# Kernel tuning notes

Measured on AMD Instinct MI355X. Metric: run time of the kernel, lower is better.

The kernel has to match this reference:

```python
import jax, jax.numpy as jnp
import numpy as np

B, N, D = 8, 8192, 256
H, DK, M, DH = 8, 32, 64, 512   # heads, per-head key dim, n_omega random features, mlp hidden
DV = D // H                      # per-head value dim
EPS = 1e-3                       # keras LayerNormalization default epsilon


def _layer_norm(x, g, b):
    mu = jnp.mean(x, axis=-1, keepdims=True)
    var = jnp.var(x, axis=-1, keepdims=True)
    return g * (x - mu) * jax.lax.rsqrt(var + EPS) + b


def _phi(x, omega):
    # Performer positive random features. x: (B,H,N,DK), omega: (DK,M)
    x = x / (DK ** 0.25)
    proj = jnp.einsum('bhnd,dm->bhnm', x, omega)
    sq = 0.5 * jnp.sum(x * x, axis=-1, keepdims=True)
    return jnp.exp(proj - sq) / jnp.sqrt(jnp.asarray(M, x.dtype))


def _mhla(x, Wq, bq, Wk, bk, Wv, bv, Wo, bo, omega):
    # x: (B,N,D). Multi-head linear (kernelized) attention.
    q = (x @ Wq + bq).reshape(B, N, H, DK).transpose(0, 2, 1, 3)  # bhnd
    k = (x @ Wk + bk).reshape(B, N, H, DK).transpose(0, 2, 1, 3)
    v = (x @ Wv + bv).reshape(B, N, H, DV).transpose(0, 2, 1, 3)
    pq = _phi(q, omega)                                   # (B,H,N,M)
    pk = _phi(k, omega)                                   # (B,H,N,M)
    kv = jnp.einsum('bhnm,bhnd->bhmd', pk, v)             # (B,H,M,DV)
    num = jnp.einsum('bhnm,bhmd->bhnd', pq, kv)           # (B,H,N,DV)
    den = jnp.einsum('bhnm,bhm->bhn', pq, jnp.sum(pk, axis=2))
    out = num / den[..., None]
    out = out.transpose(0, 2, 1, 3).reshape(B, N, D)
    return out @ Wo + bo


def _gru_gate(x, y, Wr, Ur, Wz, Uz, Wg, Ug, bg):
    # GTrXL gating: x = residual (old state), y = new sublayer output.
    r = jax.nn.sigmoid(y @ Wr + x @ Ur)
    z = jax.nn.sigmoid(y @ Wz + x @ Uz - bg)
    h = jnp.tanh(y @ Wg + (r * x) @ Ug)
    return (1.0 - z) * x + z * h


def setup_inputs() -> dict:
    key = jax.random.key(0)
    ks = iter(jax.random.split(key, 40))
    w = lambda *s: jax.random.normal(next(ks), s, jnp.float32) * 0.02
    inp = {
        'x': jax.random.normal(next(ks), (B, N, D), jnp.float32),
        'ln1_g': jnp.ones((D,), jnp.float32), 'ln1_b': jnp.zeros((D,), jnp.float32),
        'Wq': w(D, H * DK), 'bq': jnp.zeros((H * DK,), jnp.float32),
        'Wk': w(D, H * DK), 'bk': jnp.zeros((H * DK,), jnp.float32),
        'Wv': w(D, H * DV), 'bv': jnp.zeros((H * DV,), jnp.float32),
        'Wo': w(D, D), 'bo': jnp.zeros((D,), jnp.float32),
        'omega': jax.random.normal(next(ks), (DK, M), jnp.float32),
        'g1_Wr': w(D, D), 'g1_Ur': w(D, D), 'g1_Wz': w(D, D), 'g1_Uz': w(D, D),
        'g1_Wg': w(D, D), 'g1_Ug': w(D, D), 'g1_bg': 2.0 * jnp.ones((D,), jnp.float32),
        'ln2_g': jnp.ones((D,), jnp.float32), 'ln2_b': jnp.zeros((D,), jnp.float32),
        'W1': w(D, DH), 'b1': jnp.zeros((DH,), jnp.float32),
        'W2': w(DH, D), 'b2': jnp.zeros((D,), jnp.float32),
        'g2_Wr': w(D, D), 'g2_Ur': w(D, D), 'g2_Wz': w(D, D), 'g2_Uz': w(D, D),
        'g2_Wg': w(D, D), 'g2_Ug': w(D, D), 'g2_bg': 2.0 * jnp.ones((D,), jnp.float32),
    }
    return inp


def reference(x, ln1_g, ln1_b, Wq, bq, Wk, bk, Wv, bv, Wo, bo, omega,
              g1_Wr, g1_Ur, g1_Wz, g1_Uz, g1_Wg, g1_Ug, g1_bg,
              ln2_g, ln2_b, W1, b1, W2, b2,
              g2_Wr, g2_Ur, g2_Wz, g2_Uz, g2_Wg, g2_Ug, g2_bg):
    residual = x
    h = _layer_norm(x, ln1_g, ln1_b)
    h = _mhla(h, Wq, bq, Wk, bk, Wv, bv, Wo, bo, omega)
    h = _gru_gate(residual, h, g1_Wr, g1_Ur, g1_Wz, g1_Uz, g1_Wg, g1_Ug, g1_bg)
    residual = h
    h2 = _layer_norm(h, ln2_g, ln2_b)
    h2 = jax.nn.relu(h2 @ W1 + b1)
    h2 = jax.nn.relu(h2 @ W2 + b2)
    out = _gru_gate(residual, h2, g2_Wr, g2_Ur, g2_Wz, g2_Uz, g2_Wg, g2_Ug, g2_bg)
    return out
```

## Files before the change

### kernel.cpp

```cpp
#include <hip/hip_runtime.h>

#define B_ 8
#define N_ 8192
#define H_ 8
#define KSPLIT 16
#define BN 65536

typedef float f32x4 __attribute__((ext_vector_type(4)));
typedef __bf16 bf16x8 __attribute__((ext_vector_type(8)));
typedef unsigned short u16;

__device__ __forceinline__ u16 f2b(float f) {
  union { float f; unsigned u; } v; v.f = f;
  return (u16)((v.u + 0x7fffu + ((v.u >> 16) & 1u)) >> 16);
}
__device__ __forceinline__ float b2f(u16 u) {
  union { unsigned u; float f; } v; v.u = ((unsigned)u) << 16;
  return v.f;
}

__device__ __forceinline__ void gload16(const void* g, const void* lds) {
  __builtin_amdgcn_global_load_lds(
      (const __attribute__((address_space(1))) unsigned int*)(unsigned long long)g,
      (__attribute__((address_space(3))) unsigned int*)(unsigned long long)lds,
      16, 0, 0);
}

__device__ __forceinline__ void ld16f(const float* p, float* f) {
#pragma unroll
  for (int j = 0; j < 4; ++j) {
    float4 q = *(const float4*)(p + j * 4);
    f[j * 4 + 0] = q.x; f[j * 4 + 1] = q.y; f[j * 4 + 2] = q.z; f[j * 4 + 3] = q.w;
  }
}
__device__ __forceinline__ void ld16b(const u16* p, float* f) {
  uint4 a = *(const uint4*)p, b = *(const uint4*)(p + 8);
  const unsigned uu[8] = {a.x, a.y, a.z, a.w, b.x, b.y, b.z, b.w};
#pragma unroll
  for (int j = 0; j < 8; ++j) {
    f[2 * j]     = b2f((u16)(uu[j] & 0xffff));
    f[2 * j + 1] = b2f((u16)(uu[j] >> 16));
  }
}
__device__ __forceinline__ void st16b(u16* p, const float* f) {
  u16 o[16];
#pragma unroll
  for (int j = 0; j < 16; ++j) o[j] = f2b(f[j]);
  *(uint4*)p = *(const uint4*)o;
  *(uint4*)(p + 8) = *(const uint4*)(o + 8);
}
__device__ __forceinline__ void st16f(float* p, const float* f) {
#pragma unroll
  for (int j = 0; j < 4; ++j) {
    float4 q; q.x = f[j * 4]; q.y = f[j * 4 + 1]; q.z = f[j * 4 + 2]; q.w = f[j * 4 + 3];
    *(float4*)(p + j * 4) = q;
  }
}

template <int MODE, int XBF, int CF32, int BSEL>
__global__ __launch_bounds__(512) void gemm2(
    const u16* __restrict__ A1, int lda1, const u16* __restrict__ A2, int lda2,
    const u16* __restrict__ BT, int ldb,
    const float* __restrict__ bias, const void* __restrict__ auxX,
    const u16* __restrict__ auxZ, const float* __restrict__ auxS,
    void* __restrict__ Cv, void* __restrict__ Cv2, void* __restrict__ Cv3,
    int ldc, int K) {
  __shared__ __align__(16) u16 As[3][4096];
  __shared__ __align__(16) u16 Bs[3][8192];
  const int t = threadIdx.x, lane = t & 63, w = t >> 6;
  const int nwg = gridDim.x * gridDim.y;
  const int flat = blockIdx.x + gridDim.x * blockIdx.y;
  const int wg = (flat & 7) * (nwg >> 3) + (flat >> 3);
  const int bx = wg % gridDim.x, by = wg / gridDim.x;
  const int rowBase = by * 128, colBase = bx * 256;
  const int aBase = (BSEL == 2) ? (rowBase & 255) : rowBase;
  const u16* BTb = BT;
  if (BSEL == 1) BTb = BT + (size_t)(rowBase >> 13) * 131072;
  if (BSEL == 2) BTb = BT + (size_t)(rowBase >> 8) * 131072;

  const int lr = lane & 15, kg = lane >> 4;
  const int wrow = (w >> 2) * 64, wcol = (w & 3) * 64;

  f32x4 acc[4][4];
#pragma unroll
  for (int m = 0; m < 4; ++m)
#pragma unroll
    for (int n = 0; n < 4; ++n) acc[m][n] = 0.f;

  const int nt = K >> 5;
  auto stage = [&](int s) {
    const int buf = s % 3;
    const int k0 = s << 5;
    const u16* Ap; int la, ka;
    if (k0 < 256) { Ap = A1; la = lda1; ka = k0; }
    else          { Ap = A2; la = lda2; ka = k0 - 256; }
    {
      int row = t >> 2, sl = t & 3;
      int ks = (sl ^ ((row & 6) >> 1)) * 8;
      gload16(&Ap[(size_t)(aBase + row) * la + ka + ks], &As[buf][t * 8]);
    }
#pragma unroll
    for (int j = 0; j < 2; ++j) {
      int slot = j * 512 + t;
      int col = slot >> 2, sl = slot & 3;
      int ks = (sl ^ ((col & 6) >> 1)) * 8;
      gload16(&BTb[(size_t)(colBase + col) * ldb + k0 + ks], &Bs[buf][slot * 8]);
    }
  };

  auto lbar = [&]() {
    asm volatile("s_waitcnt lgkmcnt(0)" ::: "memory");
    __builtin_amdgcn_sched_barrier(0);
    __builtin_amdgcn_s_barrier();
    __builtin_amdgcn_sched_barrier(0);
  };

  stage(0);
  stage(1);
  for (int s = 0; s < nt; ++s) {
    const int buf = s % 3;
    if (nt - s > 1) asm volatile("s_waitcnt vmcnt(3)" ::: "memory");
    else            asm volatile("s_waitcnt vmcnt(0)" ::: "memory");
    __builtin_amdgcn_sched_barrier(0);
    __builtin_amdgcn_s_barrier();
    __builtin_amdgcn_sched_barrier(0);
    if (s + 2 < nt) stage(s + 2);
    bf16x8 af[4], bf[4];
#pragma unroll
    for (int m = 0; m < 4; ++m) {
      int row = wrow + m * 16 + lr;
      af[m] = *(const bf16x8*)&As[buf][row * 32 + (kg ^ ((row & 6) >> 1)) * 8];
    }
#pragma unroll
    for (int n = 0; n < 4; ++n) {
      int col = wcol + n * 16 + lr;
      bf[n] = *(const bf16x8*)&Bs[buf][col * 32 + (kg ^ ((col & 6) >> 1)) * 8];
    }
    __builtin_amdgcn_s_setprio(1);
#pragma unroll
    for (int m = 0; m < 4; ++m)
#pragma unroll
      for (int n = 0; n < 4; ++n)
        acc[m][n] = __builtin_amdgcn_mfma_f32_16x16x32_bf16(af[m], bf[n], acc[m][n], 0, 0, 0);
    __builtin_amdgcn_s_setprio(0);
  }

  lbar();
  float* scr = (float*)&Bs[0][0];
#pragma unroll
  for (int m = 0; m < 4; ++m) {
    if (m) lbar();
#pragma unroll
    for (int n = 0; n < 4; ++n)
#pragma unroll
      for (int i = 0; i < 4; ++i)
        scr[((w >> 2) * 16 + kg * 4 + i) * 260 + wcol + n * 16 + lr] = acc[m][n][i];
    lbar();
    const int sr = t >> 4, cs = (t & 15) * 16;
    const int grow = rowBase + (sr >> 4) * 64 + m * 16 + (sr & 15);
    const int gcol = colBase + cs;
    float vv[16];
#pragma unroll
    for (int j = 0; j < 4; ++j) {
      float4 q = *(const float4*)&scr[sr * 260 + cs + j * 4];
      vv[j * 4] = q.x; vv[j * 4 + 1] = q.y; vv[j * 4 + 2] = q.z; vv[j * 4 + 3] = q.w;
    }
    if (MODE == 0 || MODE == 1) {
      float bb[16]; ld16f(&bias[gcol], bb);
#pragma unroll
      for (int j = 0; j < 16; ++j) {
        vv[j] += bb[j];
        if (MODE == 1) vv[j] = fmaxf(vv[j], 0.f);
      }
      st16b(&((u16*)Cv)[(size_t)grow * ldc + gcol], vv);
    } else if (MODE == 10) {
      float bb[16]; ld16f(&bias[gcol], bb);
      float sx = auxS[(size_t)grow * 8 + (gcol >> 6)];
#pragma unroll
      for (int j = 0; j < 16; ++j) vv[j] = __expf(vv[j] + bb[j] - sx) * 0.125f;
      const float* kvf = (const float*)auxX;
      float sv[16];
      ld16f(&kvf[((size_t)(grow >> 13) * 8 + (gcol >> 6)) * 2112 + 2048 + (gcol & 63)], sv);
      float dp = 0.f;
#pragma unroll
      for (int j = 0; j < 16; ++j) dp = __fmaf_rn(vv[j], sv[j], dp);
      dp += __shfl_xor(dp, 1);
      dp += __shfl_xor(dp, 2);
      const float r = 1.0f / dp;
#pragma unroll
      for (int j = 0; j < 16; ++j) vv[j] *= r;
      st16b(&((u16*)Cv)[(size_t)grow * ldc + gcol], vv);
    } else if (MODE == 7) {
      float bb[16]; ld16f(&bias[gcol], bb);
#pragma unroll
      for (int j = 0; j < 16; ++j) vv[j] += bb[j];
      if (colBase < 512) {
        u16* Cp; int c2;
        if (colBase < 256) { Cp = (u16*)Cv;  c2 = gcol; }
        else               { Cp = (u16*)Cv2; c2 = gcol - 256; }
        st16b(&Cp[(size_t)grow * ldc + c2], vv);
      } else {
        float s = 0.f;
#pragma unroll
        for (int j = 0; j < 16; ++j) s += vv[j] * vv[j];
        s += __shfl_xor(s, 1);
        if ((t & 1) == 0)
          const_cast<float*>(auxS)[(size_t)grow * 8 + ((gcol - 512) >> 5)] =
              0.0883883476483184f * s;
      }
    } else if (MODE == 8) {
      if (colBase < 256) {
        float xv[16];
        if (XBF) ld16b(&((const u16*)auxX)[(size_t)grow * 256 + gcol], xv);
        else     ld16f(&((const float*)auxX)[(size_t)grow * 256 + gcol], xv);
#pragma unroll
        for (int j = 0; j < 16; ++j) vv[j] = (1.f / (1.f + __expf(-vv[j]))) * xv[j];
        st16b(&((u16*)Cv)[(size_t)grow * ldc + gcol], vv);
      } else {
        float bb[16]; ld16f(&bias[gcol - 256], bb);
#pragma unroll
        for (int j = 0; j < 16; ++j) vv[j] = 1.f / (1.f + __expf(-(vv[j] - bb[j])));
        st16b(&((u16*)Cv2)[(size_t)grow * ldc + gcol - 256], vv);
      }
    } else if (MODE == 4) {
      float zz[16], xv[16];
      ld16b(&auxZ[(size_t)grow * 256 + gcol], zz);
      if (XBF) ld16b(&((const u16*)auxX)[(size_t)grow * 256 + gcol], xv);
      else     ld16f(&((const float*)auxX)[(size_t)grow * 256 + gcol], xv);
#pragma unroll
      for (int j = 0; j < 16; ++j)
        vv[j] = (1.f - zz[j]) * xv[j] + zz[j] * tanhf(vv[j]);
      if (CF32) st16f(&((float*)Cv)[(size_t)grow * ldc + gcol], vv);
      else      st16b(&((u16*)Cv)[(size_t)grow * ldc + gcol], vv);
    } else if (MODE == 9) {
      float zz[16], xv[16];
      ld16b(&auxZ[(size_t)grow * 256 + gcol], zz);
      ld16b(&((const u16*)auxX)[(size_t)grow * 256 + gcol], xv);
#pragma unroll
      for (int j = 0; j < 16; ++j)
        vv[j] = (1.f - zz[j]) * xv[j] + zz[j] * tanhf(vv[j]);
      st16b(&((u16*)Cv)[(size_t)grow * 256 + gcol], vv);
      float s1 = 0.f, s2 = 0.f;
#pragma unroll
      for (int j = 0; j < 16; ++j) { s1 += vv[j]; s2 += vv[j] * vv[j]; }
#pragma unroll
      for (int off = 1; off < 16; off <<= 1) {
        s1 += __shfl_xor(s1, off);
        s2 += __shfl_xor(s2, off);
      }
      float mu = s1 * (1.f / 256.f);
      float var = s2 * (1.f / 256.f) - mu * mu;
      float rs = rsqrtf(var + 1e-3f);
      float gg[16], bb2[16];
      ld16f(&bias[gcol], gg);
      ld16f(&auxS[gcol], bb2);
#pragma unroll
      for (int j = 0; j < 16; ++j) vv[j] = gg[j] * (vv[j] - mu) * rs + bb2[j];
      st16b(&((u16*)Cv2)[(size_t)grow * 256 + gcol], vv);
    }
  }
}

__global__ __launch_bounds__(256) void fkv_kernel(const u16* __restrict__ Kb,
                                                  const u16* __restrict__ Vb,
                                                  const u16* __restrict__ omT,
                                                  float* __restrict__ part) {
  __shared__ __align__(16) char smem[33792];
  u16* Ks  = (u16*)smem;
  u16* omS = Ks + 4096;
  u16* pkT = omS + 2048;
  u16* vT  = pkT + 64 * 72;
  float* sqL = (float*)(vT + 48 * 72);
  float* red = (float*)smem;

  const int bh = blockIdx.x, split = blockIdx.y;
  const int b = bh >> 3, h = bh & 7;
  const int t = threadIdx.x, lane = t & 63, w = t >> 6;
  const int lr = lane & 15, kg = lane >> 4;
  const size_t rbase = (size_t)b * N_ + (size_t)split * (N_ / KSPLIT);

  {
    int m = t >> 2, sl = t & 3;
    gload16(&omT[m * 32 + ((sl ^ ((m & 6) >> 1)) * 8)], &omS[t * 8]);
  }
  for (int i = t; i < 16 * 128; i += 256) {
    int r = 32 + (i >> 7), tok = i & 127;
    vT[r * 72 + tok] = (r == 32) ? (u16)0x3f80 : (u16)0;
  }

  f32x4 kacc[4][3];
#pragma unroll
  for (int mi = 0; mi < 4; ++mi)
#pragma unroll
    for (int ni = 0; ni < 3; ++ni) kacc[mi][ni] = 0.f;

  for (int tile = 0; tile < (N_ / KSPLIT) / 128; ++tile) {
    __syncthreads();
    const size_t gt0 = rbase + tile * 128;
#pragma unroll
    for (int j = 0; j < 2; ++j) {
      int slot = j * 256 + t;
      int tok = slot >> 2, sl = slot & 3;
      gload16(&Kb[(gt0 + tok) * 256 + h * 32 + ((sl ^ ((tok & 6) >> 1)) * 8)],
              &Ks[slot * 8]);
    }
#pragma unroll
    for (int j = 0; j < 2; ++j) {
      int slot = j * 256 + t;
      int tok = slot >> 2, seg = slot & 3;
      uint4 q = *(const uint4*)&Vb[(gt0 + tok) * 256 + h * 32 + seg * 8];
      const unsigned uu[4] = {q.x, q.y, q.z, q.w};
#pragma unroll
      for (int jj = 0; jj < 4; ++jj) {
        vT[(seg * 8 + jj * 2 + 0) * 72 + tok] = (u16)(uu[jj] & 0xffffu);
        vT[(seg * 8 + jj * 2 + 1) * 72 + tok] = (u16)(uu[jj] >> 16);
      }
    }
    asm volatile("s_waitcnt vmcnt(0)" ::: "memory");
    __syncthreads();

    uint4 araw[2];
    bf16x8 af[2];
#pragma unroll
    for (int mi = 0; mi < 2; ++mi) {
      int row = w * 32 + mi * 16 + lr;
      araw[mi] = *(const uint4*)&Ks[row * 32 + (kg ^ ((row & 6) >> 1)) * 8];
      af[mi] = *(const bf16x8*)&araw[mi];
    }
#pragma unroll
    for (int mi = 0; mi < 2; ++mi) {
      const unsigned uu[4] = {araw[mi].x, araw[mi].y, araw[mi].z, araw[mi].w};
      float s = 0.f;
#pragma unroll
      for (int j = 0; j < 4; ++j) {
        float lo = b2f((u16)(uu[j] & 0xffffu)), hi = b2f((u16)(uu[j] >> 16));
        s = __fmaf_rn(lo, lo, s); s = __fmaf_rn(hi, hi, s);
      }
      s += __shfl_xor(s, 16);
      s += __shfl_xor(s, 32);
      if (lane < 16) sqL[w * 32 + mi * 16 + lr] = 0.0883883476483184f * s;
    }
    bf16x8 bo[4];
#pragma unroll
    for (int ni = 0; ni < 4; ++ni) {
      int col = ni * 16 + lr;
      bo[ni] = *(const bf16x8*)&omS[col * 32 + (kg ^ ((col & 6) >> 1)) * 8];
    }
    f32x4 pacc[2][4];
#pragma unroll
    for (int mi = 0; mi < 2; ++mi)
#pragma unroll
      for (int ni = 0; ni < 4; ++ni) {
        f32x4 z = 0.f;
        pacc[mi][ni] = __builtin_amdgcn_mfma_f32_16x16x32_bf16(af[mi], bo[ni], z, 0, 0, 0);
      }
    float sqv[2][4];
#pragma unroll
    for (int mi = 0; mi < 2; ++mi)
#pragma unroll
      for (int i = 0; i < 4; ++i)
        sqv[mi][i] = sqL[w * 32 + mi * 16 + kg * 4 + i];
#pragma unroll
    for (int mi = 0; mi < 2; ++mi)
#pragma unroll
      for (int ni = 0; ni < 4; ++ni) {
        u16 p4[4];
#pragma unroll
        for (int i = 0; i < 4; ++i)
          p4[i] = f2b(__expf(pacc[mi][ni][i] - sqv[mi][i]) * 0.125f);
        int m = ni * 16 + lr;
        int tok = w * 32 + mi * 16 + kg * 4;
        *(unsigned long long*)&pkT[m * 72 + tok] = *(const unsigned long long*)p4;
      }
    __syncthreads();

    {
      int ktok = w * 32;
      bf16x8 a2[4], b2v[3];
#pragma unroll
      for (int mi = 0; mi < 4; ++mi)
        a2[mi] = *(const bf16x8*)&pkT[(mi * 16 + lr) * 72 + ktok + kg * 8];
#pragma unroll
      for (int ni = 0; ni < 3; ++ni)
        b2v[ni] = *(const bf16x8*)&vT[(ni * 16 + lr) * 72 + ktok + kg * 8];
#pragma unroll
      for (int mi = 0; mi < 4; ++mi)
#pragma unroll
        for (int ni = 0; ni < 3; ++ni)
          kacc[mi][ni] = __builtin_amdgcn_mfma_f32_16x16x32_bf16(a2[mi], b2v[ni], kacc[mi][ni], 0, 0, 0);
    }
  }

  __syncthreads();
#pragma unroll
  for (int mi = 0; mi < 4; ++mi) {
#pragma unroll
    for (int ni = 0; ni < 3; ++ni) {
      if (ni < 2) {
#pragma unroll
        for (int i = 0; i < 4; ++i)
          red[w * 2112 + (mi * 16 + kg * 4 + i) * 33 + ni * 16 + lr] = kacc[mi][ni][i];
      } else if (lr == 0) {
#pragma unroll
        for (int i = 0; i < 4; ++i)
          red[w * 2112 + (mi * 16 + kg * 4 + i) * 33 + 32] = kacc[mi][2][i];
      }
    }
  }
  __syncthreads();
  float* dst = part + (size_t)(bh * KSPLIT + split) * 2112;
  for (int idx = t; idx < 2112; idx += 256) {
    int m, c;
    if (idx < 2048) { m = idx >> 5; c = idx & 31; }
    else            { m = idx - 2048; c = 32; }
    float s = 0.f;
#pragma unroll
    for (int w4 = 0; w4 < 4; ++w4) s += red[w4 * 2112 + m * 33 + c];
    dst[idx] = s;
  }
}

struct TJob { const float* s; u16* d; int lds, ldd, rows, cols; };
struct PrepArgs {
  TJob j[18];
  const float* omega; u16* wphiT; u16* omT;
  const float* bk; const float* bv; const float* bq; float* bias;
  const float* Wq; u16* WqOT; float* bqOm;
};
__global__ __launch_bounds__(256) void prep_kernel(PrepArgs P) {
  int t = threadIdx.x;
  const float SCALE = 0.4204482076268573f;
  if (blockIdx.y == 18) {
    for (int i = 0; i < 16; ++i) {
      int idx = (blockIdx.x * 256 + t) * 16 + i;
      int c = idx >> 8, k = idx & 255;
      float v = 0.f;
      if ((k >> 5) == (c >> 6)) v = P.omega[(k & 31) * 64 + (c & 63)] * SCALE;
      P.wphiT[idx] = f2b(v);
    }
    return;
  }
  if (blockIdx.y == 19) {
    if (blockIdx.x == 0) {
      for (int i = t; i < 2048; i += 256) {
        int m = i >> 5, k = i & 31;
        P.omT[i] = f2b(P.omega[k * 64 + m] * SCALE);
      }
    } else if (blockIdx.x == 1) {
      P.bias[t] = P.bk[t]; P.bias[256 + t] = P.bv[t]; P.bias[512 + t] = P.bq[t];
      P.bias[768 + t] = 0.f; P.bias[1024 + t] = 0.f;
    } else if (blockIdx.x == 2) {
      for (int c = t; c < 512; c += 256) {
        float s = 0.f;
        const int hb = (c >> 6) * 32, mm = c & 63;
        for (int d = 0; d < 32; ++d)
          s = __fmaf_rn(P.bq[hb + d], P.omega[d * 64 + mm], s);
        P.bqOm[c] = s * SCALE;
      }
    }
    return;
  }
  if (blockIdx.y == 20) {
    for (int i = 0; i < 16; ++i) {
      int idx = (blockIdx.x * 256 + t) * 16 + i;
      int c = idx >> 8, k = idx & 255;
      const int hb = (c >> 6) * 32, mm = c & 63;
      float s = 0.f;
      for (int d = 0; d < 32; ++d)
        s = __fmaf_rn(P.Wq[k * 256 + hb + d], P.omega[d * 64 + mm], s);
      P.WqOT[c * 256 + k] = f2b(s * SCALE);
    }
    return;
  }
  TJob jb = P.j[blockIdx.y];
  int ntc = jb.cols >> 6;
  int tile = blockIdx.x;
  if (tile >= (jb.rows >> 6) * ntc) return;
  int tr = (tile / ntc) << 6, tc = (tile % ntc) << 6;
  __shared__ float sm[64][68];
#pragma unroll
  for (int i = 0; i < 4; ++i) {
    int idx = t + 256 * i;
    int r = idx >> 4, c = (idx & 15) * 4;
    float4 v = *(const float4*)&jb.s[(size_t)(tr + r) * jb.lds + tc + c];
    sm[r][c] = v.x; sm[r][c + 1] = v.y; sm[r][c + 2] = v.z; sm[r][c + 3] = v.w;
  }
  __syncthreads();
#pragma unroll
  for (int i = 0; i < 4; ++i) {
    int idx = t + 256 * i;
    int c = idx >> 4, r = (idx & 15) * 4;
    ushort4 p; p.x = f2b(sm[r][c]); p.y = f2b(sm[r + 1][c]);
    p.z = f2b(sm[r + 2][c]); p.w = f2b(sm[r + 3][c]);
    *(ushort4*)&jb.d[(size_t)(tc + c) * jb.ldd + tr + r] = p;
  }
}

__global__ __launch_bounds__(256) void kvred_kernel(const float* __restrict__ part,
                                                    float* __restrict__ fin,
                                                    u16* __restrict__ kb) {
  const int bid = blockIdx.x, t = threadIdx.x;
  if (bid < 64) {
    const int bh = bid;
    for (int idx = t; idx < 2112; idx += 256) {
      float s = 0.f;
#pragma unroll
      for (int sp = 0; sp < KSPLIT; ++sp) s += part[(size_t)(bh * KSPLIT + sp) * 2112 + idx];
      fin[(size_t)bh * 2112 + idx] = s;
    }
    return;
  }
  int idx = (bid - 64) * 256 + t;
  int b = idx >> 17, rem = idx & 131071;
  int kp = rem >> 8, d = rem & 255;
  float v = 0.f;
  if ((kp >> 6) == (d >> 5)) {
    const int bh = b * 8 + (kp >> 6);
    const int off = (kp & 63) * 32 + (d & 31);
#pragma unroll
    for (int sp = 0; sp < KSPLIT; ++sp) v += part[(size_t)(bh * KSPLIT + sp) * 2112 + off];
  }
  kb[idx] = f2b(v);
}

__global__ __launch_bounds__(256) void ln_kernel3(const float* __restrict__ x,
                                                  const float* __restrict__ g,
                                                  const float* __restrict__ b,
                                                  u16* __restrict__ out,
                                                  u16* __restrict__ xb) {
  const int row = blockIdx.x * 4 + (threadIdx.x >> 6);
  const int lane = threadIdx.x & 63;
  const float4 v = *(const float4*)&x[(size_t)row * 256 + lane * 4];
  ushort4 xo;
  xo.x = f2b(v.x); xo.y = f2b(v.y); xo.z = f2b(v.z); xo.w = f2b(v.w);
  *(ushort4*)&xb[(size_t)row * 256 + lane * 4] = xo;
  float s = v.x + v.y + v.z + v.w;
  float s2 = v.x * v.x + v.y * v.y + v.z * v.z + v.w * v.w;
#pragma unroll
  for (int off = 1; off < 64; off <<= 1) {
    s += __shfl_xor(s, off);
    s2 += __shfl_xor(s2, off);
  }
  const float mu = s * (1.f / 256.f);
  const float var = s2 * (1.f / 256.f) - mu * mu;
  const float rs = rsqrtf(var + 1e-3f);
  const float4 gv = *(const float4*)&g[lane * 4];
  const float4 bv = *(const float4*)&b[lane * 4];
  ushort4 o;
  o.x = f2b(gv.x * (v.x - mu) * rs + bv.x);
  o.y = f2b(gv.y * (v.y - mu) * rs + bv.y);
  o.z = f2b(gv.z * (v.z - mu) * rs + bv.z);
  o.w = f2b(gv.w * (v.w - mu) * rs + bv.w);
  *(ushort4*)&out[(size_t)row * 256 + lane * 4] = o;
}

extern "C" void kernel_launch(void* const* d_in, const int* in_sizes, int n_in,
                              void* d_out, int out_size, void* d_ws, size_t ws_size,
                              hipStream_t stream) {
  (void)in_sizes; (void)n_in; (void)out_size; (void)ws_size;
  const float* x     = (const float*)d_in[0];
  const float* ln1_g = (const float*)d_in[1];
  const float* ln1_b = (const float*)d_in[2];
  const float* Wq    = (const float*)d_in[3];
  const float* bq    = (const float*)d_in[4];
  const float* Wk    = (const float*)d_in[5];
  const float* bk    = (const float*)d_in[6];
  const float* Wv    = (const float*)d_in[7];
  const float* bv    = (const float*)d_in[8];
  const float* Wo    = (const float*)d_in[9];
  const float* bo    = (const float*)d_in[10];
  const float* omega = (const float*)d_in[11];
  const float* g1_Wr = (const float*)d_in[12];
  const float* g1_Ur = (const float*)d_in[13];
  const float* g1_Wz = (const float*)d_in[14];
  const float* g1_Uz = (const float*)d_in[15];
  const float* g1_Wg = (const float*)d_in[16];
  const float* g1_Ug = (const float*)d_in[17];
  const float* g1_bg = (const float*)d_in[18];
  const float* ln2_g = (const float*)d_in[19];
  const float* ln2_b = (const float*)d_in[20];
  const float* W1    = (const float*)d_in[21];
  const float* b1    = (const float*)d_in[22];
  const float* W2    = (const float*)d_in[23];
  const float* b2    = (const float*)d_in[24];
  const float* g2_Wr = (const float*)d_in[25];
  const float* g2_Ur = (const float*)d_in[26];
  const float* g2_Wz = (const float*)d_in[27];
  const float* g2_Uz = (const float*)d_in[28];
  const float* g2_Wg = (const float*)d_in[29];
  const float* g2_Ug = (const float*)d_in[30];
  const float* g2_bg = (const float*)d_in[31];

  const size_t SZB = (size_t)BN * 256;
  u16* S0 = (u16*)d_ws;
  u16* S1 = S0 + SZB;
  u16* S2 = S1 + SZB;
  u16* S3 = S2 + SZB;
  u16* qkvT  = S3 + SZB;
  u16* wphiT = qkvT + 768 * 256;
  u16* woT   = wphiT + 512 * 256;
  u16* g1rzT = woT + 65536;
  u16* g1hpT = g1rzT + 262144;
  u16* w1T   = g1hpT + 131072;
  u16* w2T   = w1T + 131072;
  u16* g2rzT = w2T + 131072;
  u16* g2hpT = g2rzT + 262144;
  u16* kvbdA = g2hpT + 131072;
  u16* WoKVT = kvbdA + 1048576;
  u16* omTg  = WoKVT + 1048576;
  u16* WqOT  = omTg + 2048;
  float* bias768 = (float*)(WqOT + 131072);
  float* zero512 = bias768 + 768;
  float* bqOm    = bias768 + 1280;
  float* kvpart  = bqOm + 512;
  float* kvfin   = kvpart + (size_t)64 * KSPLIT * 2112;
  float* sqQ     = kvfin + 64 * 2112;
  u16* xb        = (u16*)(sqQ + (size_t)BN * 8);
  u16* db = (u16*)d_out;
  float* outf = (float*)d_out;

  dim3 blk(256), blkG(512);
  dim3 g1c(1, BN / 128), g2c(2, BN / 128), g3c(3, BN / 128);

  PrepArgs P;
  auto job = [](const float* s, u16* d, int lds, int ldd, int r, int c) {
    TJob t; t.s = s; t.d = d; t.lds = lds; t.ldd = ldd; t.rows = r; t.cols = c; return t;
  };
  P.j[0]  = job(Wk, qkvT, 256, 256, 256, 256);
  P.j[1]  = job(Wv, qkvT + 256 * 256, 256, 256, 256, 256);
  P.j[2]  = job(Wq, qkvT + 512 * 256, 256, 256, 256, 256);
  P.j[3]  = job(Wo, woT, 256, 256, 256, 256);
  P.j[4]  = job(g1_Wr, g1rzT, 256, 512, 256, 256);
  P.j[5]  = job(g1_Ur, g1rzT + 256, 256, 512, 256, 256);
  P.j[6]  = job(g1_Wz, g1rzT + 256 * 512, 256, 512, 256, 256);
  P.j[7]  = job(g1_Uz, g1rzT + 256 * 512 + 256, 256, 512, 256, 256);
  P.j[8]  = job(g1_Wg, g1hpT, 256, 512, 256, 256);
  P.j[9]  = job(g1_Ug, g1hpT + 256, 256, 512, 256, 256);
  P.j[10] = job(W1, w1T, 512, 256, 256, 512);
  P.j[11] = job(W2, w2T, 256, 512, 512, 256);
  P.j[12] = job(g2_Wr, g2rzT, 256, 512, 256, 256);
  P.j[13] = job(g2_Ur, g2rzT + 256, 256, 512, 256, 256);
  P.j[14] = job(g2_Wz, g2rzT + 256 * 512, 256, 512, 256, 256);
  P.j[15] = job(g2_Uz, g2rzT + 256 * 512 + 256, 256, 512, 256, 256);
  P.j[16] = job(g2_Wg, g2hpT, 256, 512, 256, 256);
  P.j[17] = job(g2_Ug, g2hpT + 256, 256, 512, 256, 256);
  P.omega = omega; P.wphiT = wphiT; P.omT = omTg;
  P.bk = bk; P.bv = bv; P.bq = bq; P.bias = bias768;
  P.Wq = Wq; P.WqOT = WqOT; P.bqOm = bqOm;
  prep_kernel<<<dim3(32, 21), blk, 0, stream>>>(P);

  ln_kernel3<<<BN / 4, blk, 0, stream>>>(x, ln1_g, ln1_b, S0, xb);
  gemm2<7,0,0,0><<<g3c, blkG, 0, stream>>>(S0, 256, S0, 256, qkvT, 256,
      bias768, nullptr, nullptr, sqQ, S1, S2, nullptr, 256, 256);
  fkv_kernel<<<dim3(64, KSPLIT), blk, 0, stream>>>(S1, S2, omTg, kvpart);
  kvred_kernel<<<4160, blk, 0, stream>>>(kvpart, kvfin, kvbdA);
  gemm2<0,0,0,2><<<dim3(2, 16), blkG, 0, stream>>>(woT, 256, woT, 256, kvbdA, 256,
      zero512, nullptr, nullptr, nullptr, WoKVT, nullptr, nullptr, 512, 256);
  gemm2<10,0,0,0><<<g2c, blkG, 0, stream>>>(S0, 256, S0, 256, WqOT, 256,
      bqOm, kvfin, nullptr, sqQ, db, nullptr, nullptr, 512, 256);
  gemm2<0,0,0,1><<<g1c, blkG, 0, stream>>>(db, 512, db + 256, 512, WoKVT, 512,
      bo, nullptr, nullptr, nullptr, S3, nullptr, nullptr, 256, 512);
  gemm2<8,1,0,0><<<g2c, blkG, 0, stream>>>(S3, 256, xb, 256, g1rzT, 512,
      g1_bg, xb, nullptr, nullptr, db, db + SZB, nullptr, 256, 512);
  gemm2<9,1,0,0><<<g1c, blkG, 0, stream>>>(S3, 256, db, 256, g1hpT, 512,
      ln2_g, xb, db + SZB, ln2_b, S3, S0, nullptr, 256, 512);
  gemm2<1,0,0,0><<<g2c, blkG, 0, stream>>>(S0, 256, S0, 256, w1T, 256,
      b1, nullptr, nullptr, nullptr, db, nullptr, nullptr, 512, 256);
  gemm2<1,0,0,0><<<g1c, blkG, 0, stream>>>(db, 512, db + 256, 512, w2T, 512,
      b2, nullptr, nullptr, nullptr, S1, nullptr, nullptr, 256, 512);
  gemm2<8,1,0,0><<<g2c, blkG, 0, stream>>>(S1, 256, S3, 256, g2rzT, 512,
      g2_bg, S3, nullptr, nullptr, S2, S0, nullptr, 256, 512);
  gemm2<4,1,1,0><<<g1c, blkG, 0, stream>>>(S1, 256, S2, 256, g2hpT, 512,
      nullptr, S3, S0, nullptr, outf, nullptr, nullptr, 256, 512);
}
```

Before: 542.7 us.

## Enlarge GEMM tile to 256x256 with split-K double-buffered LDS pipeline

The shared GEMM kernel now computes 256x256 output tiles per 512-thread workgroup instead of 128x256, so each wave holds 8x4 accumulator fragments. Each 64-wide K step is loaded as two 32-wide halves into a double-buffered LDS layout, and A and B prefetches are interleaved between the two M-halves of the MFMA work. The goal is more reuse per loaded byte and better overlap of global loads with MFMA. In exchange it doubles the accumulator registers, raises LDS use, adds extra barriers, and halves the number of workgroups per GEMM, which may lower occupancy and leave more of the GPU idle.

```diff
diff --git a/kernel.cpp b/kernel.cpp
--- a/kernel.cpp
+++ b/kernel.cpp
@@ -65,99 +65,124 @@
     const u16* __restrict__ auxZ, const float* __restrict__ auxS,
     void* __restrict__ Cv, void* __restrict__ Cv2, void* __restrict__ Cv3,
     int ldc, int K) {
-  __shared__ __align__(16) u16 As[3][4096];
-  __shared__ __align__(16) u16 Bs[3][8192];
+  __shared__ __align__(16) u16 As[2][2][8192];
+  __shared__ __align__(16) u16 Bs[2][2][8192];
   const int t = threadIdx.x, lane = t & 63, w = t >> 6;
   const int nwg = gridDim.x * gridDim.y;
   const int flat = blockIdx.x + gridDim.x * blockIdx.y;
   const int wg = (flat & 7) * (nwg >> 3) + (flat >> 3);
   const int bx = wg % gridDim.x, by = wg / gridDim.x;
-  const int rowBase = by * 128, colBase = bx * 256;
-  const int aBase = (BSEL == 2) ? (rowBase & 255) : rowBase;
+  const int rowBase = by * 256, colBase = bx * 256;
+  const int aBase = (BSEL == 2) ? 0 : rowBase;
   const u16* BTb = BT;
   if (BSEL == 1) BTb = BT + (size_t)(rowBase >> 13) * 131072;
   if (BSEL == 2) BTb = BT + (size_t)(rowBase >> 8) * 131072;
 
   const int lr = lane & 15, kg = lane >> 4;
-  const int wrow = (w >> 2) * 64, wcol = (w & 3) * 64;
-
-  f32x4 acc[4][4];
-#pragma unroll
-  for (int m = 0; m < 4; ++m)
+  const int wrow = (w >> 2) * 128, wcol = (w & 3) * 64;
+
+  f32x4 acc[8][4];
+#pragma unroll
+  for (int m = 0; m < 8; ++m)
 #pragma unroll
     for (int n = 0; n < 4; ++n) acc[m][n] = 0.f;
 
-  const int nt = K >> 5;
-  auto stage = [&](int s) {
-    const int buf = s % 3;
-    const int k0 = s << 5;
+  const int NT = K >> 6;
+  const int NH = NT * 2;
+
+  auto stageA = [&](int H) {
+    const int tile = H >> 1, kh = H & 1, buf = tile & 1;
+    const int k0 = tile * 64 + kh * 32;
     const u16* Ap; int la, ka;
     if (k0 < 256) { Ap = A1; la = lda1; ka = k0; }
     else          { Ap = A2; la = lda2; ka = k0 - 256; }
-    {
-      int row = t >> 2, sl = t & 3;
-      int ks = (sl ^ ((row & 6) >> 1)) * 8;
-      gload16(&Ap[(size_t)(aBase + row) * la + ka + ks], &As[buf][t * 8]);
-    }
 #pragma unroll
     for (int j = 0; j < 2; ++j) {
-      int slot = j * 512 + t;
-      int col = slot >> 2, sl = slot & 3;
-      int ks = (sl ^ ((col & 6) >> 1)) * 8;
-      gload16(&BTb[(size_t)(colBase + col) * ldb + k0 + ks], &Bs[buf][slot * 8]);
+      int g = j * 512 + t;
+      int row = g >> 2, sl = g & 3;
+      gload16(&Ap[(size_t)(aBase + row) * la + ka + (sl ^ ((row & 6) >> 1)) * 8],
+              &As[buf][kh][g * 8]);
     }
   };
-
-  auto lbar = [&]() {
-    asm volatile("s_waitcnt lgkmcnt(0)" ::: "memory");
+  auto stageB = [&](int H) {
+    const int tile = H >> 1, kh = H & 1, buf = tile & 1;
+    const int k0 = tile * 64 + kh * 32;
+#pragma unroll
+    for (int j = 0; j < 2; ++j) {
+      int g = j * 512 + t;
+      int col = g >> 2, sl = g & 3;
+      gload16(&BTb[(size_t)(colBase + col) * ldb + k0 + (sl ^ ((col & 6) >> 1)) * 8],
+              &Bs[buf][kh][g * 8]);
+    }
+  };
+
+  auto sbar = [&]() {
     __builtin_amdgcn_sched_barrier(0);
     __builtin_amdgcn_s_barrier();
     __builtin_amdgcn_sched_barrier(0);
   };
 
-  stage(0);
-  stage(1);
-  for (int s = 0; s < nt; ++s) {
-    const int buf = s % 3;
-    if (nt - s > 1) asm volatile("s_waitcnt vmcnt(3)" ::: "memory");
-    else            asm volatile("s_waitcnt vmcnt(0)" ::: "memory");
-    __builtin_amdgcn_sched_barrier(0);
-    __builtin_amdgcn_s_barrier();
-    __builtin_amdgcn_sched_barrier(0);
-    if (s + 2 < nt) stage(s + 2);
-    bf16x8 af[4], bf[4];
-#pragma unroll
-    for (int m = 0; m < 4; ++m) {
-      int row = wrow + m * 16 + lr;
-      af[m] = *(const bf16x8*)&As[buf][row * 32 + (kg ^ ((row & 6) >> 1)) * 8];
-    }
-#pragma unroll
-    for (int n = 0; n < 4; ++n) {
-      int col = wcol + n * 16 + lr;
-      bf[n] = *(const bf16x8*)&Bs[buf][col * 32 + (kg ^ ((col & 6) >> 1)) * 8];
-    }
-    __builtin_amdgcn_s_setprio(1);
-#pragma unroll
-    for (int m = 0; m < 4; ++m)
-#pragma unroll
-      for (int n = 0; n < 4; ++n)
-        acc[m][n] = __builtin_amdgcn_mfma_f32_16x16x32_bf16(af[m], bf[n], acc[m][n], 0, 0, 0);
-    __builtin_amdgcn_s_setprio(0);
-  }
-
-  lbar();
-  float* scr = (float*)&Bs[0][0];
-#pragma unroll
-  for (int m = 0; m < 4; ++m) {
-    if (m) lbar();
+  stageA(0); stageB(0);
+  stageA(1); stageB(1);
+  asm volatile("s_waitcnt vmcnt(4)" ::: "memory");
+  sbar();
+
+  for (int h = 0; h < NH; ++h) {
+    const int tile = h >> 1, kh = h & 1, buf = tile & 1;
+#pragma unroll
+    for (int mh = 0; mh < 2; ++mh) {
+      bf16x8 af[4], bf[4];
+#pragma unroll
+      for (int i = 0; i < 4; ++i) {
+        int r = wrow + mh * 64 + i * 16 + lr;
+        af[i] = *(const bf16x8*)&As[buf][kh][r * 32 + (kg ^ ((r & 6) >> 1)) * 8];
+      }
+#pragma unroll
+      for (int n = 0; n < 4; ++n) {
+        int c = wcol + n * 16 + lr;
+        bf[n] = *(const bf16x8*)&Bs[buf][kh][c * 32 + (kg ^ ((c & 6) >> 1)) * 8];
+      }
+      if (h + 2 < NH) {
+        if (mh == 0) stageA(h + 2);
+        else         stageB(h + 2);
+      }
+      sbar();
+      asm volatile("s_waitcnt lgkmcnt(0)" ::: "memory");
+      __builtin_amdgcn_sched_barrier(0);
+      __builtin_amdgcn_s_setprio(1);
+#pragma unroll
+      for (int m = 0; m < 4; ++m)
+#pragma unroll
+        for (int n = 0; n < 4; ++n)
+          acc[mh * 4 + m][n] =
+              __builtin_amdgcn_mfma_f32_16x16x32_bf16(af[m], bf[n], acc[mh * 4 + m][n], 0, 0, 0);
+      __builtin_amdgcn_s_setprio(0);
+      if (mh == 1 && h + 1 < NH) {
+        if (h + 2 < NH) asm volatile("s_waitcnt vmcnt(4)" ::: "memory");
+        else            asm volatile("s_waitcnt vmcnt(0)" ::: "memory");
+      }
+      sbar();
+    }
+  }
+
+  asm volatile("s_waitcnt vmcnt(0) lgkmcnt(0)" ::: "memory");
+  sbar();
+  float* scr = (float*)&As[0][0][0];
+#pragma unroll
+  for (int mf = 0; mf < 8; ++mf) {
+    if (mf) {
+      asm volatile("s_waitcnt lgkmcnt(0)" ::: "memory");
+      sbar();
+    }
 #pragma unroll
     for (int n = 0; n < 4; ++n)
 #pragma unroll
       for (int i = 0; i < 4; ++i)
-        scr[((w >> 2) * 16 + kg * 4 + i) * 260 + wcol + n * 16 + lr] = acc[m][n][i];
-    lbar();
+        scr[((w >> 2) * 16 + kg * 4 + i) * 260 + wcol + n * 16 + lr] = acc[mf][n][i];
+    asm volatile("s_waitcnt lgkmcnt(0)" ::: "memory");
+    sbar();
     const int sr = t >> 4, cs = (t & 15) * 16;
-    const int grow = rowBase + (sr >> 4) * 64 + m * 16 + (sr & 15);
+    const int grow = rowBase + (sr >> 4) * 128 + mf * 16 + (sr & 15);
     const int gcol = colBase + cs;
     float vv[16];
 #pragma unroll
@@ -620,7 +645,7 @@
   float* outf = (float*)d_out;
 
   dim3 blk(256), blkG(512);
-  dim3 g1c(1, BN / 128), g2c(2, BN / 128), g3c(3, BN / 128);
+  dim3 g1c(1, BN / 256), g2c(2, BN / 256), g3c(3, BN / 256);
 
   PrepArgs P;
   auto job = [](const float* s, u16* d, int lds, int ldd, int r, int c) {
@@ -654,7 +679,7 @@
       bias768, nullptr, nullptr, sqQ, S1, S2, nullptr, 256, 256);
   fkv_kernel<<<dim3(64, KSPLIT), blk, 0, stream>>>(S1, S2, omTg, kvpart);
   kvred_kernel<<<4160, blk, 0, stream>>>(kvpart, kvfin, kvbdA);
-  gemm2<0,0,0,2><<<dim3(2, 16), blkG, 0, stream>>>(woT, 256, woT, 256, kvbdA, 256,
+  gemm2<0,0,0,2><<<dim3(2, 8), blkG, 0, stream>>>(woT, 256, woT, 256, kvbdA, 256,
       zero512, nullptr, nullptr, nullptr, WoKVT, nullptr, nullptr, 512, 256);
   gemm2<10,0,0,0><<<g2c, blkG, 0, stream>>>(S0, 256, S0, 256, WqOT, 256,
       bqOm, kvfin, nullptr, sqQ, db, nullptr, nullptr, 512, 256);
```

After: 779.4 us. 1.44x slower.
